# Kernel tuning notes

Hardware: AMD Instinct MI355X
Metric: run time of the kernel (lower is better)

Reference implementation:

```python
import jax, jax.numpy as jnp
import numpy as np

N_NODES = 100000
N_EDGES = 1600000
D_IN = 64
D_OUT = 64


def setup_inputs() -> dict:
    key = jax.random.key(0)
    k_x, k_e, k_wl, k_bl, k_wr = jax.random.split(key, 5)
    x = jax.random.normal(k_x, (N_NODES, D_IN), dtype=jnp.float32)
    edge_index = jax.random.randint(k_e, (2, N_EDGES), 0, N_NODES, dtype=jnp.int64)
    W_l = jax.random.normal(k_wl, (D_IN, D_OUT), dtype=jnp.float32) / np.sqrt(D_IN)
    b_l = jax.random.normal(k_bl, (D_OUT,), dtype=jnp.float32) * 0.01
    W_r = jax.random.normal(k_wr, (D_IN, D_OUT), dtype=jnp.float32) / np.sqrt(D_IN)
    return {"x": x, "edge_index": edge_index, "W_l": W_l, "b_l": b_l, "W_r": W_r}


def reference(x, edge_index, W_l, b_l, W_r):
    # SAGEConv (mean aggregation) + ReLU:
    #   out_i = relu( W_l^T mean_{j->i} x_j + b_l + W_r^T x_i )
    n = x.shape[0]
    src, dst = edge_index[0], edge_index[1]
    # gather source features and mean-aggregate into destination nodes
    agg = jax.ops.segment_sum(x[src], dst, num_segments=n)           # [N, D_IN]
    cnt = jax.ops.segment_sum(jnp.ones_like(dst, dtype=x.dtype), dst, num_segments=n)
    mean_nbr = agg / jnp.maximum(cnt, 1.0)[:, None]                   # [N, D_IN]
    out = mean_nbr @ W_l + b_l + x @ W_r                              # [N, D_OUT]
    return jax.nn.relu(out)
```

## Files before the change

kernel.cpp:

```cpp
#include <hip/hip_runtime.h>

#define N_NODES 100000
#define N_EDGES 1600000
#define D 64
#define NBKT 391
#define REG 5120
#define SCB 1024
#define A_I4 1024
#define N_I4 (N_EDGES / 4)
#define TBC 10

typedef __attribute__((ext_vector_type(8))) short bf16x8;
typedef __attribute__((ext_vector_type(4))) float f32x4;

__device__ __forceinline__ unsigned short f2bf(float f) {
    union { float f; unsigned u; } v; v.f = f;
    unsigned r = v.u + 0x7FFFu + ((v.u >> 16) & 1u);
    return (unsigned short)(r >> 16);
}

#define CVT_ITEMS ((N_NODES * D) / 4)
#define CVT_BLKS 1563
__global__ __launch_bounds__(SCB) void scatter_cvt(const float* __restrict__ x,
                                                   unsigned* __restrict__ xq,
                                                   const int* __restrict__ ei,
                                                   unsigned* __restrict__ fc,
                                                   unsigned* __restrict__ bpairs) {
    __shared__ unsigned hc[NBKT];
    __shared__ unsigned hb[NBKT];
    const int blk = blockIdx.x;
    const int tid = threadIdx.x;
    if (blk < NBKT) {
        if (tid < NBKT) hc[tid] = 0;
        __syncthreads();

        const int g = blk * A_I4 + tid;
        const int4* sptr = (const int4*)ei;
        const int4* dptr = (const int4*)(ei + N_EDGES);

        unsigned pay[4];
        unsigned meta[4];
        if (g < N_I4) {
            int4 s4 = sptr[g];
            int4 d4 = dptr[g];
            const int dd[4] = { d4.x, d4.y, d4.z, d4.w };
            const int ss[4] = { s4.x, s4.y, s4.z, s4.w };
            #pragma unroll
            for (int c = 0; c < 4; ++c) {
                const unsigned b = (unsigned)dd[c] >> 8;
                const unsigned lr = atomicAdd(&hc[b], 1u);
                meta[c] = (b << 13) | lr;
                pay[c]  = ((unsigned)ss[c] << 8) | ((unsigned)dd[c] & 255u);
            }
        } else {
            #pragma unroll
            for (int c = 0; c < 4; ++c) meta[c] = 0xFFFFFFFFu;
        }
        __syncthreads();
        if (tid < NBKT) {
            unsigned c = hc[tid];
            if (c) hb[tid] = atomicAdd(&fc[tid], c);
        }
        __syncthreads();
        #pragma unroll
        for (int e = 0; e < 4; ++e) {
            if (meta[e] != 0xFFFFFFFFu) {
                const unsigned b   = meta[e] >> 13;
                const unsigned lr  = meta[e] & 0x1FFFu;
                const unsigned pos = hb[b] + lr;
                if (pos < REG) bpairs[(size_t)b * REG + pos] = pay[e];
            }
        }
    } else {
        const int j = (blk - NBKT) * SCB + tid;
        if (j < CVT_ITEMS) {
            float4 v = ((const float4*)x)[j];
            unsigned u = __builtin_amdgcn_cvt_pk_fp8_f32(v.x, v.y, 0u, false);
            u = __builtin_amdgcn_cvt_pk_fp8_f32(v.z, v.w, u, true);
            xq[j] = u;
        }
    }
}

#define STEPF(SI, J, N, A0, A1, A2, A3)                                      \
    {                                                                         \
        _Pragma("unroll")                                                     \
        for (int t_ = 0; t_ < 4; ++t_) {                                      \
            const int e_  = (J) + 4 * t_;                                     \
            const int sel_ = __shfl((SI), e_ + grp, 64);                      \
            unsigned v_ = xq32[(size_t)sel_ * 16 + lq];                       \
            v_ = (e_ + grp < (N)) ? v_ : 0u;                                  \
            (A0) += __builtin_amdgcn_cvt_f32_fp8(v_, 0);                      \
            (A1) += __builtin_amdgcn_cvt_f32_fp8(v_, 1);                      \
            (A2) += __builtin_amdgcn_cvt_f32_fp8(v_, 2);                      \
            (A3) += __builtin_amdgcn_cvt_f32_fp8(v_, 3);                      \
        }                                                                     \
    }

#define TAILF(S0, DD, A0, A1, A2, A3)                                        \
    for (int b2_ = 64; b2_ < (DD); b2_ += 64) {                              \
        const int n2_ = ((DD) - b2_ < 64) ? ((DD) - b2_) : 64;               \
        const int cl2_ = (lane < n2_) ? lane : (n2_ - 1);                    \
        const int sit_ = csrL[(S0) + b2_ + cl2_];                            \
        for (int j_ = 0; j_ < n2_; j_ += 16) {                               \
            STEPF(sit_, j_, n2_, A0, A1, A2, A3)                             \
        }                                                                     \
    }

#define FINR(R, DV, A0, A1, A2, A3)                                          \
    {                                                                         \
        (A0) += __shfl_xor((A0), 16, 64); (A0) += __shfl_xor((A0), 32, 64);   \
        (A1) += __shfl_xor((A1), 16, 64); (A1) += __shfl_xor((A1), 32, 64);   \
        (A2) += __shfl_xor((A2), 16, 64); (A2) += __shfl_xor((A2), 32, 64);   \
        (A3) += __shfl_xor((A3), 16, 64); (A3) += __shfl_xor((A3), 32, 64);   \
        const float inv_ = 1.0f / fmaxf((float)(DV), 1.0f);                   \
        if (lane < 16) {                                                      \
            const unsigned m0_ = ((unsigned)f2bf((A1) * inv_) << 16)          \
                                 | f2bf((A0) * inv_);                         \
            const unsigned m1_ = ((unsigned)f2bf((A3) * inv_) << 16)          \
                                 | f2bf((A2) * inv_);                         \
            const int sw_ = ((R) & 7) << 2;                                   \
            sAw[((R) * 64 + 2 * lane) ^ sw_]     = m0_;                       \
            sAw[((R) * 64 + 2 * lane + 1) ^ sw_] = m1_;                       \
        }                                                                     \
    }

#define SBLK 512
__global__ __launch_bounds__(SBLK) void sage_kernel(const float* __restrict__ x,
                                                    const unsigned* __restrict__ xq32,
                                                    const unsigned* __restrict__ fc,
                                                    const unsigned* __restrict__ bpairs,
                                                    const float* __restrict__ Wl,
                                                    const float* __restrict__ bl,
                                                    const float* __restrict__ Wr,
                                                    float* __restrict__ out) {
    __shared__ unsigned short sWt[D * 2 * D];
    __shared__ float sbl[D];
    __shared__ int csrL[REG];
    __shared__ unsigned sdeg[256];
    __shared__ unsigned soff[256];
    __shared__ unsigned sscan[256];
    __shared__ unsigned sA32[(SBLK / 64) * 16 * 64];

    const int b   = blockIdx.x;
    const int tid = threadIdx.x;

    for (int i = tid; i < D * D; i += SBLK) {
        int k = i >> 6, c = i & 63;
        int swz = (c & 7) << 3;
        sWt[(c * 128 + k) ^ swz]      = f2bf(Wl[i]);
        sWt[(c * 128 + 64 + k) ^ swz] = f2bf(Wr[i]);
    }
    if (tid < D) sbl[tid] = bl[tid];
    if (tid < 256) sdeg[tid] = 0;
    __syncthreads();

    unsigned cnt = fc[b];
    if (cnt > REG) cnt = REG;
    unsigned pk[TBC];
    unsigned rk[TBC];
    #pragma unroll
    for (int t = 0; t < TBC; ++t) {
        const unsigned i = (unsigned)tid + t * (unsigned)SBLK;
        if (i < cnt) {
            const unsigned p = bpairs[(size_t)b * REG + i];
            pk[t] = p;
            rk[t] = atomicAdd(&sdeg[p & 255u], 1u);
        } else {
            pk[t] = 0xFFFFFFFFu;
        }
    }
    __syncthreads();
    unsigned v = 0;
    if (tid < 256) { v = sdeg[tid]; sscan[tid] = v; }
    __syncthreads();
    for (int off = 1; off < 256; off <<= 1) {
        unsigned u = 0;
        if (tid < 256 && tid >= off) u = sscan[tid - off];
        __syncthreads();
        if (tid < 256) sscan[tid] += u;
        __syncthreads();
    }
    if (tid < 256) soff[tid] = sscan[tid] - v;
    __syncthreads();
    #pragma unroll
    for (int t = 0; t < TBC; ++t) {
        if (pk[t] != 0xFFFFFFFFu) {
            const unsigned p  = pk[t];
            const unsigned dl = p & 255u;
            csrL[soff[dl] + rk[t]] = (int)(p >> 8);
        }
    }
    __syncthreads();

    const int lane = tid & 63;
    const int wib  = tid >> 6;
    unsigned int* sAw = sA32 + wib * (16 * 64);
    const int grp = lane >> 4;
    const int lq  = lane & 15;

    for (int h = 0; h < 2; ++h) {
        const int loc0  = wib * 32 + h * 16;
        const int node0 = b * 256 + loc0;
        if (node0 >= N_NODES) break;

        {
            const float2* __restrict__ x2 = (const float2*)x;
            const int c = lane & 31;
            #pragma unroll
            for (int rr = 0; rr < 8; ++rr) {
                const int r = 2 * rr + (lane >> 5);
                float2 vv = x2[(size_t)(node0 + r) * 32 + c];
                const unsigned mp = ((unsigned)f2bf(vv.y) << 16) | f2bf(vv.x);
                sAw[(r * 64 + 32 + c) ^ ((r & 7) << 2)] = mp;
            }
        }

        const int l16  = lane & 15;
        const int offl = (int)((sdeg[loc0 + l16] << 13) | soff[loc0 + l16]);

        int si[16];
        int dg[16];
        #pragma unroll
        for (int r = 0; r < 16; ++r) {
            const int er = __builtin_amdgcn_readlane(offl, r);
            const int d  = (int)((unsigned)er >> 13);
            dg[r] = d;
            const int s0 = er & 0x1FFF;
            const int dm = (d > 0) ? d : 1;
            const int cl = (lane < dm) ? lane : (dm - 1);
            si[r] = csrL[s0 + cl];
        }

        #pragma unroll
        for (int p = 0; p < 8; ++p) {
            const int rA = 2 * p, rB = 2 * p + 1;
            const int dA = dg[rA], dB = dg[rB];
            const int nA = (dA < 64) ? dA : 64;
            const int nB = (dB < 64) ? dB : 64;

            float a0 = 0.0f, a1 = 0.0f, a2 = 0.0f, a3 = 0.0f;
            float b0 = 0.0f, b1 = 0.0f, b2 = 0.0f, b3 = 0.0f;
            int jA = 0, jB = 0;
            while (jA < nA && jB < nB) {
                STEPF(si[rA], jA, nA, a0, a1, a2, a3)
                STEPF(si[rB], jB, nB, b0, b1, b2, b3)
                jA += 16; jB += 16;
            }
            while (jA < nA) { STEPF(si[rA], jA, nA, a0, a1, a2, a3) jA += 16; }
            while (jB < nB) { STEPF(si[rB], jB, nB, b0, b1, b2, b3) jB += 16; }
            if (dA > 64) {
                const int s0A = __builtin_amdgcn_readlane(offl, rA) & 0x1FFF;
                TAILF(s0A, dA, a0, a1, a2, a3)
            }
            if (dB > 64) {
                const int s0B = __builtin_amdgcn_readlane(offl, rB) & 0x1FFF;
                TAILF(s0B, dB, b0, b1, b2, b3)
            }

            FINR(rA, dA, a0, a1, a2, a3)
            FINR(rB, dB, b0, b1, b2, b3)
        }

        const unsigned short* sAu = (const unsigned short*)sAw;
        const int row = lane & 15;
        const int kb  = lane >> 4;

        bf16x8 afr[4];
        #pragma unroll
        for (int kc = 0; kc < 4; ++kc) {
            int us = (row * 128 + kc * 32 + kb * 8) ^ ((row & 7) << 3);
            afr[kc] = *(const bf16x8*)(sAu + us);
        }

        #pragma unroll
        for (int ct = 0; ct < 4; ++ct) {
            const int col = ct * 16 + row;
            f32x4 acc = {0.0f, 0.0f, 0.0f, 0.0f};
            #pragma unroll
            for (int kc = 0; kc < 4; ++kc) {
                int us = (col * 128 + kc * 32 + kb * 8) ^ ((col & 7) << 3);
                bf16x8 bfr = *(const bf16x8*)(sWt + us);
                acc = __builtin_amdgcn_mfma_f32_16x16x32_bf16(afr[kc], bfr, acc, 0, 0, 0);
            }
            const float bias = sbl[col];
            const int crow0 = (lane >> 4) * 4;
            #pragma unroll
            for (int i = 0; i < 4; ++i) {
                out[(node0 + crow0 + i) * D + col] = fmaxf(acc[i] + bias, 0.0f);
            }
        }
    }
}

extern "C" void kernel_launch(void* const* d_in, const int* in_sizes, int n_in,
                              void* d_out, int out_size, void* d_ws, size_t ws_size,
                              hipStream_t stream) {
    const float* x  = (const float*)d_in[0];
    const int*   ei = (const int*)d_in[1];
    const float* Wl = (const float*)d_in[2];
    const float* bl = (const float*)d_in[3];
    const float* Wr = (const float*)d_in[4];
    float* out = (float*)d_out;

    unsigned* xq      = (unsigned*)d_ws;
    unsigned* fc      = xq + (size_t)N_NODES * 16;
    unsigned* bpairs  = fc + 512;

    hipMemsetAsync(fc, 0, 512 * sizeof(unsigned), stream);

    scatter_cvt<<<NBKT + CVT_BLKS, SCB, 0, stream>>>(x, xq, ei, fc, bpairs);

    sage_kernel<<<NBKT, SBLK, 0, stream>>>(x, xq, fc, bpairs, Wl, bl, Wr, out);
}
```

Measured before the change: 77.51 us.

## Stage bucketed edge scatter in LDS to coalesce global writes

Each scatter block now runs an exclusive prefix scan over its per-bucket counts, sorts its edge payloads into shared memory by bucket, then writes them out in contiguous order. Consecutive threads then write consecutive positions within a bucket's region instead of scattering randomly across hundreds of buckets. This is meant to cut uncoalesced global stores. In exchange it adds a 9-step barrier-based scan, extra LDS traffic and roughly 25 KB more shared memory per block, which may lower occupancy.

```diff
diff --git a/kernel.cpp b/kernel.cpp
--- a/kernel.cpp
+++ b/kernel.cpp
@@ -28,6 +28,11 @@
                                                    unsigned* __restrict__ bpairs) {
     __shared__ unsigned hc[NBKT];
     __shared__ unsigned hb[NBKT];
+    __shared__ unsigned lb[NBKT];
+    __shared__ unsigned sscan[512];
+    __shared__ unsigned lbTot;
+    __shared__ unsigned spay[4096];
+    __shared__ unsigned short sbkt[4096];
     const int blk = blockIdx.x;
     const int tid = threadIdx.x;
     if (blk < NBKT) {
@@ -39,8 +44,10 @@
         const int4* dptr = (const int4*)(ei + N_EDGES);
 
         unsigned pay[4];
-        unsigned meta[4];
-        if (g < N_I4) {
+        unsigned bkt[4];
+        unsigned lr[4];
+        bool valid = (g < N_I4);
+        if (valid) {
             int4 s4 = sptr[g];
             int4 d4 = dptr[g];
             const int dd[4] = { d4.x, d4.y, d4.z, d4.w };
@@ -48,28 +55,43 @@
             #pragma unroll
             for (int c = 0; c < 4; ++c) {
                 const unsigned b = (unsigned)dd[c] >> 8;
-                const unsigned lr = atomicAdd(&hc[b], 1u);
-                meta[c] = (b << 13) | lr;
-                pay[c]  = ((unsigned)ss[c] << 8) | ((unsigned)dd[c] & 255u);
-            }
-        } else {
-            #pragma unroll
-            for (int c = 0; c < 4; ++c) meta[c] = 0xFFFFFFFFu;
+                bkt[c] = b;
+                lr[c]  = atomicAdd(&hc[b], 1u);
+                pay[c] = ((unsigned)ss[c] << 8) | ((unsigned)dd[c] & 255u);
+            }
         }
         __syncthreads();
         if (tid < NBKT) {
             unsigned c = hc[tid];
-            if (c) hb[tid] = atomicAdd(&fc[tid], c);
-        }
-        __syncthreads();
-        #pragma unroll
-        for (int e = 0; e < 4; ++e) {
-            if (meta[e] != 0xFFFFFFFFu) {
-                const unsigned b   = meta[e] >> 13;
-                const unsigned lr  = meta[e] & 0x1FFFu;
-                const unsigned pos = hb[b] + lr;
-                if (pos < REG) bpairs[(size_t)b * REG + pos] = pay[e];
-            }
+            hb[tid] = c ? atomicAdd(&fc[tid], c) : 0u;
+        }
+        unsigned v = 0;
+        if (tid < 512) { v = (tid < NBKT) ? hc[tid] : 0u; sscan[tid] = v; }
+        __syncthreads();
+        for (int off = 1; off < 512; off <<= 1) {
+            unsigned u = 0;
+            if (tid < 512 && tid >= off) u = sscan[tid - off];
+            __syncthreads();
+            if (tid < 512) sscan[tid] += u;
+            __syncthreads();
+        }
+        if (tid < NBKT) lb[tid] = sscan[tid] - v;
+        if (tid == NBKT - 1) lbTot = sscan[tid];
+        __syncthreads();
+        if (valid) {
+            #pragma unroll
+            for (int c = 0; c < 4; ++c) {
+                const unsigned pos = lb[bkt[c]] + lr[c];
+                spay[pos] = pay[c];
+                sbkt[pos] = (unsigned short)bkt[c];
+            }
+        }
+        __syncthreads();
+        const unsigned total = lbTot;
+        for (unsigned i = tid; i < total; i += SCB) {
+            const unsigned b2   = sbkt[i];
+            const unsigned gpos = hb[b2] + i - lb[b2];
+            if (gpos < REG) bpairs[(size_t)b2 * REG + gpos] = spay[i];
         }
     } else {
         const int j = (blk - NBKT) * SCB + tid;
```

After: 74.29 us, median of 2. -4.2%, faster.
